# Kernel tuning notes

Hardware: AMD Instinct MI355X
Metric: run time of the kernel (lower is better)

The kernel has to match this reference:

```python
import jax, jax.numpy as jnp
import numpy as np

NUM_MEMORIES = 4096
HIDDEN_DIM = 64
TEMPERATURE = 0.5
SHRINK_THRES = 0.0025
EPS = 1e-12


def _l2_normalize(v, axis=-1):
    # matches torch F.normalize: v / max(||v||_2, eps)
    n = jnp.sqrt(jnp.sum(v * v, axis=axis, keepdims=True))
    return v / jnp.maximum(n, EPS)


def _hard_shrink_relu(w, lambd):
    # relu(w - lambd) * w / (|w - lambd| + eps)
    d = w - lambd
    return jax.nn.relu(d) * w / (jnp.abs(d) + EPS)


def setup_inputs() -> dict:
    key = jax.random.key(0)
    kx, km = jax.random.split(key)
    x = jax.random.normal(kx, (16, 2048, HIDDEN_DIM), dtype=jnp.float32)
    # xavier_uniform for (num_memories, hidden_dim)
    bound = float(np.sqrt(6.0 / (NUM_MEMORIES + HIDDEN_DIM)))
    memories = jax.random.uniform(km, (NUM_MEMORIES, HIDDEN_DIM), dtype=jnp.float32,
                                  minval=-bound, maxval=bound)
    return {"x": x, "memories": memories}


def reference(x, memories):
    # cosine similarity addressing
    x_n = _l2_normalize(x, axis=-1)                      # [B,S,D]
    m_n = _l2_normalize(memories, axis=-1)               # [M,D]
    logits = jnp.einsum('bsd,md->bsm', x_n, m_n)         # [B,S,M]
    weight = jax.nn.softmax(logits / TEMPERATURE, axis=-1)
    # hard-shrink sparsification + L1 renormalization
    weight = _hard_shrink_relu(weight, SHRINK_THRES)
    l1 = jnp.sum(jnp.abs(weight), axis=-1, keepdims=True)
    weight = weight / jnp.maximum(l1, EPS)
    read = jnp.einsum('bsm,md->bsd', weight, memories)   # [B,S,D]
    return read, weight
```

## Files before the change

### kernel.cpp

```cpp
#include <hip/hip_runtime.h>
#include <hip/hip_bf16.h>


#define NM 4096
#define HD 64
#define NROWS 32768

typedef short bf16x8 __attribute__((ext_vector_type(8)));
typedef float f32x4  __attribute__((ext_vector_type(4)));

__global__ __launch_bounds__(256) void prep_rows(const float* __restrict__ src,
                                                 ushort* __restrict__ dst,
                                                 float scale) {
    const int wave = threadIdx.x >> 6, lane = threadIdx.x & 63;
    const long row = (long)blockIdx.x * 4 + wave;
    float v = src[row * HD + lane];
    float s = v * v;
#pragma unroll
    for (int o = 32; o; o >>= 1) s += __shfl_xor(s, o, 64);
    const float inv = scale / fmaxf(sqrtf(s), 1e-12f);
    __hip_bfloat16 h = __float2bfloat16(v * inv);
    dst[row * HD + lane] = *reinterpret_cast<ushort*>(&h);
}

__global__ __launch_bounds__(256) void prep_m_swz(const float* __restrict__ mem,
                                                  ushort* __restrict__ mbs) {
    const int wave = threadIdx.x >> 6, lane = threadIdx.x & 63;
    const int row = blockIdx.x * 4 + wave;
    float v = mem[row * HD + lane];
    float s = v * v;
#pragma unroll
    for (int o = 32; o; o >>= 1) s += __shfl_xor(s, o, 64);
    const float inv = 1.0f / fmaxf(sqrtf(s), 1e-12f);
    __hip_bfloat16 h = __float2bfloat16(v * inv);
    const int t = row >> 4, c = row & 15;
    const int k = lane;
    const int f = k >> 5, q = (k >> 3) & 3, j = k & 7;
    mbs[(long)t * 1024 + f * 512 + (q * 16 + c) * 8 + j] =
        *reinterpret_cast<ushort*>(&h);
}

__global__ __launch_bounds__(256, 4) void k_fused(const ushort* __restrict__ xb,
                                                  const ushort* __restrict__ mbs,
                                                  const float* __restrict__ mem,
                                                  float* __restrict__ out_w,
                                                  float* __restrict__ out_read) {
    const int tid = threadIdx.x;
    const int wv = tid >> 6, lane = tid & 63;
    const int q = lane >> 4, c = lane & 15;
    const int m0 = blockIdx.x * 16;
    const int nbase = wv * 1024;

    __shared__ float sS[4][16];
    __shared__ float sL[4][16];
    __shared__ uint  sD[4];
    __shared__ float sred[4][16][64];

    const bf16x8 a0 = *(const bf16x8*)(xb + (long)(m0 + c) * HD + q * 8);
    const bf16x8 a1 = *(const bf16x8*)(xb + (long)(m0 + c) * HD + q * 8 + 32);
    const ushort* mstrip = mbs + (long)(wv * 64) * 1024;
    const float4 z4 = make_float4(0.0f, 0.0f, 0.0f, 0.0f);
    float4* zbase = (float4*)(out_w + (long)m0 * NM);

    float tmax8[8];
    float sm[4] = {0.0f, 0.0f, 0.0f, 0.0f};
    for (int g = 0; g < 8; g++) {
        float tm = -1e30f;
#pragma unroll 4
        for (int ii = 0; ii < 8; ii++) {
            const int i = g * 8 + ii;
            const ushort* mc = mstrip + (long)i * 1024 + lane * 8;
            const bf16x8 b0 = *(const bf16x8*)(mc);
            const bf16x8 b1 = *(const bf16x8*)(mc + 512);
            zbase[(long)i * 256 + tid] = z4;
            f32x4 t = {0.0f, 0.0f, 0.0f, 0.0f};
            t = __builtin_amdgcn_mfma_f32_16x16x32_bf16(a0, b0, t, 0, 0, 0);
            t = __builtin_amdgcn_mfma_f32_16x16x32_bf16(a1, b1, t, 0, 0, 0);
            tm = fmaxf(tm, fmaxf(fmaxf(t[0], t[1]), fmaxf(t[2], t[3])));
#pragma unroll
            for (int r = 0; r < 4; r++) sm[r] += __expf(t[r]);
        }
        tmax8[g] = tm;
    }
#pragma unroll
    for (int o = 1; o < 16; o <<= 1)
#pragma unroll
        for (int r = 0; r < 4; r++) sm[r] += __shfl_xor(sm[r], o, 64);
    if (c == 0)
#pragma unroll
        for (int r = 0; r < 4; r++) sS[wv][q * 4 + r] = sm[r];
    __asm__ volatile("s_waitcnt lgkmcnt(0)\n\ts_barrier" ::: "memory");
    float rS[4], tmin = 1e30f;
#pragma unroll
    for (int r = 0; r < 4; r++) {
        const float S = sS[0][q * 4 + r] + sS[1][q * 4 + r] +
                        sS[2][q * 4 + r] + sS[3][q * 4 + r];
        rS[r] = 1.0f / S;
        const float tau = __logf(0.0025f * S) - 1e-3f;
        tmin = fminf(tmin, tau);
    }

    uint dmask = 0;
#pragma unroll
    for (int g = 0; g < 8; g++)
        if (__ballot(tmax8[g] > tmin)) dmask |= 1u << g;
    if (lane == 0) sD[wv] = dmask;
    __asm__ volatile("s_waitcnt lgkmcnt(0)\n\ts_barrier" ::: "memory");
    const uint anyd = sD[0] | sD[1] | sD[2] | sD[3];

    if (!anyd) {
        ((float4*)(out_read + (long)m0 * HD))[tid] = z4;
        return;
    }

    __syncthreads();

    float l1[4] = {0.0f, 0.0f, 0.0f, 0.0f};
    for (int g = 0; g < 8; g++) {
        if (!((dmask >> g) & 1u)) continue;
        for (int ii = 0; ii < 8; ii++) {
            const int i = g * 8 + ii;
            const ushort* mc = mstrip + (long)i * 1024 + lane * 8;
            const bf16x8 b0 = *(const bf16x8*)(mc);
            const bf16x8 b1 = *(const bf16x8*)(mc + 512);
            f32x4 t = {0.0f, 0.0f, 0.0f, 0.0f};
            t = __builtin_amdgcn_mfma_f32_16x16x32_bf16(a0, b0, t, 0, 0, 0);
            t = __builtin_amdgcn_mfma_f32_16x16x32_bf16(a1, b1, t, 0, 0, 0);
#pragma unroll
            for (int r = 0; r < 4; r++) {
                float w = __expf(t[r]) * rS[r];
                float d = w - 0.0025f;
                l1[r] += __fdividef(fmaxf(d, 0.0f) * w, fabsf(d) + 1e-12f);
            }
        }
    }
#pragma unroll
    for (int o = 1; o < 16; o <<= 1)
#pragma unroll
        for (int r = 0; r < 4; r++) l1[r] += __shfl_xor(l1[r], o, 64);
    if (c == 0)
#pragma unroll
        for (int r = 0; r < 4; r++) sL[wv][q * 4 + r] = l1[r];
    __syncthreads();
    float rL[4];
#pragma unroll
    for (int r = 0; r < 4; r++)
        rL[r] = 1.0f / fmaxf(sL[0][q * 4 + r] + sL[1][q * 4 + r] +
                             sL[2][q * 4 + r] + sL[3][q * 4 + r], 1e-12f);

    float racc[16];
#pragma unroll
    for (int r = 0; r < 16; r++) racc[r] = 0.0f;
    float* wbase = out_w + (long)(m0 + q * 4) * NM + c;
    for (int i = 0; i < 64; i++) {
        const int n0 = nbase + i * 16;
        const ushort* mc = mstrip + (long)i * 1024 + lane * 8;
        const bf16x8 b0 = *(const bf16x8*)(mc);
        const bf16x8 b1 = *(const bf16x8*)(mc + 512);
        f32x4 t = {0.0f, 0.0f, 0.0f, 0.0f};
        t = __builtin_amdgcn_mfma_f32_16x16x32_bf16(a0, b0, t, 0, 0, 0);
        t = __builtin_amdgcn_mfma_f32_16x16x32_bf16(a1, b1, t, 0, 0, 0);
        float wf[4];
#pragma unroll
        for (int r = 0; r < 4; r++) {
            float w  = __expf(t[r]) * rS[r];
            float d  = w - 0.0025f;
            float sh = __fdividef(fmaxf(d, 0.0f) * w, fabsf(d) + 1e-12f);
            wf[r] = sh * rL[r];
            wbase[(long)r * NM + n0] = wf[r];
        }
        const bool nz = (wf[0] != 0.0f) | (wf[1] != 0.0f) |
                        (wf[2] != 0.0f) | (wf[3] != 0.0f);
        unsigned long long mask = __ballot(nz);
        while (mask) {
            const int j = __ffsll((long long)mask) - 1;
            mask &= (mask - 1);
            const int qj = j >> 4, cj = j & 15;
            float b0v = __shfl(wf[0], j, 64), b1v = __shfl(wf[1], j, 64);
            float b2v = __shfl(wf[2], j, 64), b3v = __shfl(wf[3], j, 64);
            const float mv = mem[(long)(n0 + cj) * HD + lane];
            switch (qj) {
                case 0: racc[0]  += b0v * mv; racc[1]  += b1v * mv;
                        racc[2]  += b2v * mv; racc[3]  += b3v * mv; break;
                case 1: racc[4]  += b0v * mv; racc[5]  += b1v * mv;
                        racc[6]  += b2v * mv; racc[7]  += b3v * mv; break;
                case 2: racc[8]  += b0v * mv; racc[9]  += b1v * mv;
                        racc[10] += b2v * mv; racc[11] += b3v * mv; break;
                default: racc[12] += b0v * mv; racc[13] += b1v * mv;
                         racc[14] += b2v * mv; racc[15] += b3v * mv; break;
            }
        }
    }

#pragma unroll
    for (int r = 0; r < 16; r++) sred[wv][r][lane] = racc[r];
    __syncthreads();
#pragma unroll
    for (int rr = 0; rr < 4; rr++) {
        const int row = wv * 4 + rr;
        const float v = sred[0][row][lane] + sred[1][row][lane] +
                        sred[2][row][lane] + sred[3][row][lane];
        out_read[(long)(m0 + row) * HD + lane] = v;
    }
}

extern "C" void kernel_launch(void* const* d_in, const int* in_sizes, int n_in,
                              void* d_out, int out_size, void* d_ws, size_t ws_size,
                              hipStream_t stream) {
    const float* x   = (const float*)d_in[0];
    const float* mem = (const float*)d_in[1];
    ushort* xb       = (ushort*)d_ws;
    ushort* mbs      = xb + (long)NROWS * HD;
    float* out_read  = (float*)d_out;
    float* out_w     = out_read + (long)NROWS * HD;

    prep_rows<<<NROWS / 4, 256, 0, stream>>>(x, xb, 2.0f);
    prep_m_swz<<<NM / 4, 256, 0, stream>>>(mem, mbs);
    k_fused<<<NROWS / 16, 256, 0, stream>>>(xb, mbs, mem, out_w, out_read);
}
```

Baseline: 542.5 us.

## Split fused kernel into stats/zero pass and sparse fix-up pass

```diff
diff --git a/kernel.cpp b/kernel.cpp
--- a/kernel.cpp
+++ b/kernel.cpp
@@ -40,27 +40,24 @@
         *reinterpret_cast<ushort*>(&h);
 }
 
-__global__ __launch_bounds__(256, 4) void k_fused(const ushort* __restrict__ xb,
-                                                  const ushort* __restrict__ mbs,
-                                                  const float* __restrict__ mem,
-                                                  float* __restrict__ out_w,
-                                                  float* __restrict__ out_read) {
+__global__ __launch_bounds__(256, 8) void k_main(const ushort* __restrict__ xb,
+                                                 const ushort* __restrict__ mbs,
+                                                 float* __restrict__ stats,
+                                                 uint* __restrict__ masks,
+                                                 float* __restrict__ out_w,
+                                                 float* __restrict__ out_read) {
     const int tid = threadIdx.x;
     const int wv = tid >> 6, lane = tid & 63;
     const int q = lane >> 4, c = lane & 15;
     const int m0 = blockIdx.x * 16;
-    const int nbase = wv * 1024;
 
     __shared__ float sS[4][16];
-    __shared__ float sL[4][16];
-    __shared__ uint  sD[4];
-    __shared__ float sred[4][16][64];
 
     const bf16x8 a0 = *(const bf16x8*)(xb + (long)(m0 + c) * HD + q * 8);
     const bf16x8 a1 = *(const bf16x8*)(xb + (long)(m0 + c) * HD + q * 8 + 32);
     const ushort* mstrip = mbs + (long)(wv * 64) * 1024;
+    float4* zbase = (float4*)(out_w + (long)m0 * NM);
     const float4 z4 = make_float4(0.0f, 0.0f, 0.0f, 0.0f);
-    float4* zbase = (float4*)(out_w + (long)m0 * NM);
 
     float tmax8[8];
     float sm[4] = {0.0f, 0.0f, 0.0f, 0.0f};
@@ -72,7 +69,7 @@
             const ushort* mc = mstrip + (long)i * 1024 + lane * 8;
             const bf16x8 b0 = *(const bf16x8*)(mc);
             const bf16x8 b1 = *(const bf16x8*)(mc + 512);
-            zbase[(long)i * 256 + tid] = z4;
+            zbase[i * 256 + tid] = z4;
             f32x4 t = {0.0f, 0.0f, 0.0f, 0.0f};
             t = __builtin_amdgcn_mfma_f32_16x16x32_bf16(a0, b0, t, 0, 0, 0);
             t = __builtin_amdgcn_mfma_f32_16x16x32_bf16(a1, b1, t, 0, 0, 0);
@@ -90,30 +87,52 @@
 #pragma unroll
         for (int r = 0; r < 4; r++) sS[wv][q * 4 + r] = sm[r];
     __asm__ volatile("s_waitcnt lgkmcnt(0)\n\ts_barrier" ::: "memory");
-    float rS[4], tmin = 1e30f;
+
+    float Sr[4], tmin = 1e30f;
 #pragma unroll
     for (int r = 0; r < 4; r++) {
         const float S = sS[0][q * 4 + r] + sS[1][q * 4 + r] +
                         sS[2][q * 4 + r] + sS[3][q * 4 + r];
-        rS[r] = 1.0f / S;
-        const float tau = __logf(0.0025f * S) - 1e-3f;
-        tmin = fminf(tmin, tau);
-    }
-
+        Sr[r] = S;
+        tmin = fminf(tmin, __logf(0.0025f * S) - 1e-3f);
+    }
     uint dmask = 0;
 #pragma unroll
     for (int g = 0; g < 8; g++)
         if (__ballot(tmax8[g] > tmin)) dmask |= 1u << g;
-    if (lane == 0) sD[wv] = dmask;
-    __asm__ volatile("s_waitcnt lgkmcnt(0)\n\ts_barrier" ::: "memory");
-    const uint anyd = sD[0] | sD[1] | sD[2] | sD[3];
-
-    if (!anyd) {
-        ((float4*)(out_read + (long)m0 * HD))[tid] = z4;
-        return;
-    }
-
+    if (lane == 0) masks[blockIdx.x * 4 + wv] = dmask;
+    if (wv == 0 && c == 0)
+#pragma unroll
+        for (int r = 0; r < 4; r++) stats[m0 + q * 4 + r] = Sr[r];
+    ((float4*)(out_read + (long)m0 * HD))[tid] = z4;
+}
+
+__global__ __launch_bounds__(256) void k_fix(const ushort* __restrict__ xb,
+                                             const ushort* __restrict__ mbs,
+                                             const float* __restrict__ mem,
+                                             const float* __restrict__ stats,
+                                             const uint* __restrict__ masks,
+                                             float* __restrict__ out_w,
+                                             float* __restrict__ out_read) {
+    const int tid = threadIdx.x;
+    const int wv = tid >> 6, lane = tid & 63;
+    const int q = lane >> 4, c = lane & 15;
+    const int m0 = blockIdx.x * 16;
+
+    __shared__ uint  sM[4];
+    __shared__ float sL[4][16];
+
+    if (lane == 0) sM[wv] = masks[blockIdx.x * 4 + wv];
     __syncthreads();
+    if (!(sM[0] | sM[1] | sM[2] | sM[3])) return;
+
+    const uint dmask = sM[wv];
+    const bf16x8 a0 = *(const bf16x8*)(xb + (long)(m0 + c) * HD + q * 8);
+    const bf16x8 a1 = *(const bf16x8*)(xb + (long)(m0 + c) * HD + q * 8 + 32);
+    const ushort* mstrip = mbs + (long)(wv * 64) * 1024;
+    float rS[4];
+#pragma unroll
+    for (int r = 0; r < 4; r++) rS[r] = 1.0f / stats[m0 + q * 4 + r];
 
     float l1[4] = {0.0f, 0.0f, 0.0f, 0.0f};
     for (int g = 0; g < 8; g++) {
@@ -151,56 +170,56 @@
     float racc[16];
 #pragma unroll
     for (int r = 0; r < 16; r++) racc[r] = 0.0f;
+    bool anyr = false;
     float* wbase = out_w + (long)(m0 + q * 4) * NM + c;
-    for (int i = 0; i < 64; i++) {
-        const int n0 = nbase + i * 16;
-        const ushort* mc = mstrip + (long)i * 1024 + lane * 8;
-        const bf16x8 b0 = *(const bf16x8*)(mc);
-        const bf16x8 b1 = *(const bf16x8*)(mc + 512);
-        f32x4 t = {0.0f, 0.0f, 0.0f, 0.0f};
-        t = __builtin_amdgcn_mfma_f32_16x16x32_bf16(a0, b0, t, 0, 0, 0);
-        t = __builtin_amdgcn_mfma_f32_16x16x32_bf16(a1, b1, t, 0, 0, 0);
-        float wf[4];
-#pragma unroll
-        for (int r = 0; r < 4; r++) {
-            float w  = __expf(t[r]) * rS[r];
-            float d  = w - 0.0025f;
-            float sh = __fdividef(fmaxf(d, 0.0f) * w, fabsf(d) + 1e-12f);
-            wf[r] = sh * rL[r];
-            wbase[(long)r * NM + n0] = wf[r];
-        }
-        const bool nz = (wf[0] != 0.0f) | (wf[1] != 0.0f) |
-                        (wf[2] != 0.0f) | (wf[3] != 0.0f);
-        unsigned long long mask = __ballot(nz);
-        while (mask) {
-            const int j = __ffsll((long long)mask) - 1;
-            mask &= (mask - 1);
-            const int qj = j >> 4, cj = j & 15;
-            float b0v = __shfl(wf[0], j, 64), b1v = __shfl(wf[1], j, 64);
-            float b2v = __shfl(wf[2], j, 64), b3v = __shfl(wf[3], j, 64);
-            const float mv = mem[(long)(n0 + cj) * HD + lane];
-            switch (qj) {
-                case 0: racc[0]  += b0v * mv; racc[1]  += b1v * mv;
-                        racc[2]  += b2v * mv; racc[3]  += b3v * mv; break;
-                case 1: racc[4]  += b0v * mv; racc[5]  += b1v * mv;
-                        racc[6]  += b2v * mv; racc[7]  += b3v * mv; break;
-                case 2: racc[8]  += b0v * mv; racc[9]  += b1v * mv;
-                        racc[10] += b2v * mv; racc[11] += b3v * mv; break;
-                default: racc[12] += b0v * mv; racc[13] += b1v * mv;
-                         racc[14] += b2v * mv; racc[15] += b3v * mv; break;
+    for (int g = 0; g < 8; g++) {
+        if (!((dmask >> g) & 1u)) continue;
+        for (int ii = 0; ii < 8; ii++) {
+            const int i = g * 8 + ii;
+            const int n0 = wv * 1024 + i * 16;
+            const ushort* mc = mstrip + (long)i * 1024 + lane * 8;
+            const bf16x8 b0 = *(const bf16x8*)(mc);
+            const bf16x8 b1 = *(const bf16x8*)(mc + 512);
+            f32x4 t = {0.0f, 0.0f, 0.0f, 0.0f};
+            t = __builtin_amdgcn_mfma_f32_16x16x32_bf16(a0, b0, t, 0, 0, 0);
+            t = __builtin_amdgcn_mfma_f32_16x16x32_bf16(a1, b1, t, 0, 0, 0);
+            float wf[4];
+#pragma unroll
+            for (int r = 0; r < 4; r++) {
+                float w  = __expf(t[r]) * rS[r];
+                float d  = w - 0.0025f;
+                float sh = __fdividef(fmaxf(d, 0.0f) * w, fabsf(d) + 1e-12f);
+                wf[r] = sh * rL[r];
+                wbase[(long)r * NM + n0] = wf[r];
+            }
+            const bool nz = (wf[0] != 0.0f) | (wf[1] != 0.0f) |
+                            (wf[2] != 0.0f) | (wf[3] != 0.0f);
+            unsigned long long mask = __ballot(nz);
+            if (mask) anyr = true;
+            while (mask) {
+                const int j = __ffsll((long long)mask) - 1;
+                mask &= (mask - 1);
+                const int qj = j >> 4, cj = j & 15;
+                float b0v = __shfl(wf[0], j, 64), b1v = __shfl(wf[1], j, 64);
+                float b2v = __shfl(wf[2], j, 64), b3v = __shfl(wf[3], j, 64);
+                const float mv = mem[(long)(n0 + cj) * HD + lane];
+                switch (qj) {
+                    case 0: racc[0]  += b0v * mv; racc[1]  += b1v * mv;
+                            racc[2]  += b2v * mv; racc[3]  += b3v * mv; break;
+                    case 1: racc[4]  += b0v * mv; racc[5]  += b1v * mv;
+                            racc[6]  += b2v * mv; racc[7]  += b3v * mv; break;
+                    case 2: racc[8]  += b0v * mv; racc[9]  += b1v * mv;
+                            racc[10] += b2v * mv; racc[11] += b3v * mv; break;
+                    default: racc[12] += b0v * mv; racc[13] += b1v * mv;
+                             racc[14] += b2v * mv; racc[15] += b3v * mv; break;
+                }
             }
         }
     }
-
-#pragma unroll
-    for (int r = 0; r < 16; r++) sred[wv][r][lane] = racc[r];
-    __syncthreads();
-#pragma unroll
-    for (int rr = 0; rr < 4; rr++) {
-        const int row = wv * 4 + rr;
-        const float v = sred[0][row][lane] + sred[1][row][lane] +
-                        sred[2][row][lane] + sred[3][row][lane];
-        out_read[(long)(m0 + row) * HD + lane] = v;
+    if (anyr) {
+#pragma unroll
+        for (int r = 0; r < 16; r++)
+            atomicAdd(out_read + (long)(m0 + r) * HD + lane, racc[r]);
     }
 }
 
@@ -211,10 +230,13 @@
     const float* mem = (const float*)d_in[1];
     ushort* xb       = (ushort*)d_ws;
     ushort* mbs      = xb + (long)NROWS * HD;
+    float*  stats    = (float*)(mbs + (long)NM * HD);
+    uint*   masks    = (uint*)(stats + NROWS);
     float* out_read  = (float*)d_out;
     float* out_w     = out_read + (long)NROWS * HD;
 
     prep_rows<<<NROWS / 4, 256, 0, stream>>>(x, xb, 2.0f);
     prep_m_swz<<<NM / 4, 256, 0, stream>>>(mem, mbs);
-    k_fused<<<NROWS / 16, 256, 0, stream>>>(xb, mbs, mem, out_w, out_read);
-}
+    k_main<<<NROWS / 16, 256, 0, stream>>>(xb, mbs, stats, masks, out_w, out_read);
+    k_fix<<<NROWS / 16, 256, 0, stream>>>(xb, mbs, mem, stats, masks, out_w, out_read);
+}
```

Result: no change. 549.7 us (+1.3%).
